# Kernel tuning notes

Hardware: AMD Instinct MI355X
Metric: run time of the kernel (lower is better)

The kernel has to match this reference:

```python
import jax, jax.numpy as jnp
import numpy as np

N_NODES = 50000
N_EDGES = 1_600_000
IN_CH, HID_CH, NUM_CLS = 256, 128, 64
THRESHOLD = 0.5  # default forward arg


def setup_inputs() -> dict:
    key = jax.random.key(0)
    k1, k2, k3, k4 = jax.random.split(key, 4)
    x = jax.random.normal(k1, (N_NODES, IN_CH), dtype=jnp.float32)
    edge_index = jax.random.randint(k2, (2, N_EDGES), 0, N_NODES, dtype=jnp.int32)
    W1 = jax.random.normal(k3, (IN_CH, HID_CH), dtype=jnp.float32) * (1.0 / np.sqrt(IN_CH))
    b1 = jnp.zeros((HID_CH,), dtype=jnp.float32)
    W2 = jax.random.normal(k4, (HID_CH, NUM_CLS), dtype=jnp.float32) * (1.0 / np.sqrt(HID_CH))
    b2 = jnp.zeros((NUM_CLS,), dtype=jnp.float32)
    return {"x": x, "edge_index": edge_index, "W1": W1, "b1": b1, "W2": W2, "b2": b2}


def gcn_conv(x, edge_index, W, b):
    """PyG GCNConv: add self-loops, symmetric D^-1/2 (A+I) D^-1/2 normalization,
    linear transform then gather -> weight -> segment-sum scatter, bias after agg."""
    n = x.shape[0]
    loop = jnp.arange(n, dtype=edge_index.dtype)
    src = jnp.concatenate([edge_index[0], loop])  # message source j
    dst = jnp.concatenate([edge_index[1], loop])  # aggregation target i
    deg = jax.ops.segment_sum(jnp.ones_like(src, dtype=x.dtype), dst, num_segments=n)
    dinv = jnp.where(deg > 0, jax.lax.rsqrt(deg), 0.0)
    norm = dinv[src] * dinv[dst]                  # [E+N]
    h = x @ W                                     # [N, out]
    msg = h[src] * norm[:, None]                  # [E+N, out] gather + scale
    agg = jax.ops.segment_sum(msg, dst, num_segments=n)  # scatter-add
    return agg + b


def reference(x, edge_index, W1, b1, W2, b2):
    h = jax.nn.relu(gcn_conv(x, edge_index, W1, b1))
    logits = gcn_conv(h, edge_index, W2, b2)
    probabilities = jax.nn.sigmoid(logits)
    predictions = (probabilities > THRESHOLD).astype(probabilities.dtype)
    return predictions, probabilities
```

## Files before the change

kernel.cpp:

```cpp
#include <hip/hip_runtime.h>
#include <math.h>

#define EPT 16
#define CHUNK (256 * EPT)
#define CAP 12288


__global__ void bucket_scatter_k(const int* __restrict__ src, const int* __restrict__ dst,
                                 int* __restrict__ bfill, unsigned int* __restrict__ bpk,
                                 int E) {
    __shared__ int hist[256], gofs[256], lfill[256];
    int t = threadIdx.x;
    int base = blockIdx.x * CHUNK;
    hist[t] = 0;
    lfill[t] = 0;
    __syncthreads();
    int ds[EPT], ss[EPT];
#pragma unroll
    for (int i = 0; i < EPT; ++i) {
        int e = base + i * 256 + t;
        if (e < E) {
            ds[i] = dst[e];
            ss[i] = src[e];
            atomicAdd(&hist[ds[i] >> 8], 1);
        } else {
            ds[i] = -1;
        }
    }
    __syncthreads();
    if (hist[t]) gofs[t] = atomicAdd(&bfill[t], hist[t]);
    __syncthreads();
#pragma unroll
    for (int i = 0; i < EPT; ++i) {
        if (ds[i] >= 0) {
            int b = ds[i] >> 8;
            int p = atomicAdd(&lfill[b], 1);
            int idx = gofs[b] + p;
            if (idx < CAP)
                bpk[b * CAP + idx] = ((unsigned)(ds[i] & 255) << 16) | (unsigned)ss[i];
        }
    }
}

__global__ void bucket_build_k(const unsigned int* __restrict__ bpk,
                               const int* __restrict__ bfill,
                               unsigned short* __restrict__ csr,
                               int* __restrict__ rbeg, int* __restrict__ rend,
                               float* __restrict__ dinv, int n) {
    __shared__ int hist[256], loff[256], lfill[256], tmp[256];
    __shared__ unsigned short scsr[CAP];
    int b = blockIdx.x, t = threadIdx.x;
    int base = b * CAP;
    int bsize = min(bfill[b], CAP);
    hist[t] = 0;
    lfill[t] = 0;
    __syncthreads();
    for (int idx = t; idx < bsize; idx += 256)
        atomicAdd(&hist[bpk[base + idx] >> 16], 1);
    __syncthreads();
    int deg = hist[t];
    tmp[t] = deg;
    __syncthreads();
    for (int off = 1; off < 256; off <<= 1) {
        int a = (t >= off) ? tmp[t - off] : 0;
        __syncthreads();
        tmp[t] += a;
        __syncthreads();
    }
    loff[t] = tmp[t] - deg;
    int node = (b << 8) + t;
    if (node < n) {
        rbeg[node] = base + loff[t];
        rend[node] = base + loff[t] + deg;
        dinv[node] = rsqrtf((float)(deg + 1));
    }
    __syncthreads();
    for (int idx = t; idx < bsize; idx += 256) {
        unsigned u = bpk[base + idx];
        int ln = (int)(u >> 16);
        int sp = atomicAdd(&lfill[ln], 1);
        scsr[loff[ln] + sp] = (unsigned short)(u & 0xFFFFu);
    }
    __syncthreads();
    for (int idx = t; idx < bsize; idx += 256)
        csr[base + idx] = scsr[idx];
}


__global__ __launch_bounds__(256) void gemm1_k(const float* __restrict__ x,
                                               const float* __restrict__ W,
                                               const float* __restrict__ dinv,
                                               float* __restrict__ hs, int n) {
    __shared__ float xs[32][32];
    __shared__ float ws[32][128];
    int tid = threadIdx.x;
    int cg = tid & 31;
    int rg = tid >> 5;
    int r0 = blockIdx.x * 32;
    float acc[4][4];
#pragma unroll
    for (int r = 0; r < 4; ++r)
#pragma unroll
        for (int c = 0; c < 4; ++c) acc[r][c] = 0.0f;

    for (int kc = 0; kc < 8; ++kc) {
        __syncthreads();
        {
            int v = tid;
            int r = v >> 3, k4 = v & 7;
            int row = r0 + r;
            float4 val = make_float4(0.f, 0.f, 0.f, 0.f);
            if (row < n) val = *(const float4*)(x + (long long)row * 256 + kc * 32 + k4 * 4);
            *(float4*)&xs[r][k4 * 4] = val;
        }
        {
            const float4* wg = (const float4*)(W + (long long)(kc * 32) * 128);
            float4* wsv = (float4*)&ws[0][0];
#pragma unroll
            for (int v = tid; v < 1024; v += 256) wsv[v] = wg[v];
        }
        __syncthreads();
#pragma unroll
        for (int k4 = 0; k4 < 8; ++k4) {
            float4 w0 = *(const float4*)&ws[k4 * 4 + 0][cg * 4];
            float4 w1 = *(const float4*)&ws[k4 * 4 + 1][cg * 4];
            float4 w2 = *(const float4*)&ws[k4 * 4 + 2][cg * 4];
            float4 w3 = *(const float4*)&ws[k4 * 4 + 3][cg * 4];
#pragma unroll
            for (int r = 0; r < 4; ++r) {
                float4 xv = *(const float4*)&xs[rg * 4 + r][k4 * 4];
                acc[r][0] += xv.x * w0.x + xv.y * w1.x + xv.z * w2.x + xv.w * w3.x;
                acc[r][1] += xv.x * w0.y + xv.y * w1.y + xv.z * w2.y + xv.w * w3.y;
                acc[r][2] += xv.x * w0.z + xv.y * w1.z + xv.z * w2.z + xv.w * w3.z;
                acc[r][3] += xv.x * w0.w + xv.y * w1.w + xv.z * w2.w + xv.w * w3.w;
            }
        }
    }
#pragma unroll
    for (int r = 0; r < 4; ++r) {
        int row = r0 + rg * 4 + r;
        if (row < n) {
            float di = dinv[row];
            float4 o = make_float4(acc[r][0] * di, acc[r][1] * di,
                                   acc[r][2] * di, acc[r][3] * di);
            *(float4*)(hs + (long long)row * 128 + cg * 4) = o;
        }
    }
}


__global__ __launch_bounds__(128) void gemm2_k(const float* __restrict__ h1,
                                               const float* __restrict__ W,
                                               const float* __restrict__ dinv,
                                               float* __restrict__ hs2, int n) {
    __shared__ float xs[32][64];
    int tid = threadIdx.x;
    int cg = tid & 15;
    int rg = tid >> 4;
    int r0 = blockIdx.x * 32;
    float acc[4][4];
#pragma unroll
    for (int r = 0; r < 4; ++r)
#pragma unroll
        for (int c = 0; c < 4; ++c) acc[r][c] = 0.0f;

    for (int kc = 0; kc < 2; ++kc) {
        __syncthreads();
        for (int v = tid; v < 32 * 16; v += 128) {
            int r = v >> 4;
            int k4 = v & 15;
            float4 val = make_float4(0.f, 0.f, 0.f, 0.f);
            int row = r0 + r;
            if (row < n) val = *(const float4*)(h1 + (long long)row * 128 + kc * 64 + k4 * 4);
            *(float4*)&xs[r][k4 * 4] = val;
        }
        __syncthreads();
        const float* Wp = W + (long long)(kc * 64) * 64 + cg * 4;
#pragma unroll 4
        for (int k4 = 0; k4 < 16; ++k4) {
            float4 w0 = *(const float4*)(Wp + (k4 * 4 + 0) * 64);
            float4 w1 = *(const float4*)(Wp + (k4 * 4 + 1) * 64);
            float4 w2 = *(const float4*)(Wp + (k4 * 4 + 2) * 64);
            float4 w3 = *(const float4*)(Wp + (k4 * 4 + 3) * 64);
#pragma unroll
            for (int r = 0; r < 4; ++r) {
                float4 xv = *(const float4*)&xs[rg * 4 + r][k4 * 4];
                acc[r][0] += xv.x * w0.x + xv.y * w1.x + xv.z * w2.x + xv.w * w3.x;
                acc[r][1] += xv.x * w0.y + xv.y * w1.y + xv.z * w2.y + xv.w * w3.y;
                acc[r][2] += xv.x * w0.z + xv.y * w1.z + xv.z * w2.z + xv.w * w3.z;
                acc[r][3] += xv.x * w0.w + xv.y * w1.w + xv.z * w2.w + xv.w * w3.w;
            }
        }
    }
#pragma unroll
    for (int r = 0; r < 4; ++r) {
        int row = r0 + rg * 4 + r;
        if (row < n) {
            float di = dinv[row];
            float4 o = make_float4(acc[r][0] * di, acc[r][1] * di,
                                   acc[r][2] * di, acc[r][3] * di);
            *(float4*)(hs2 + (long long)row * 64 + cg * 4) = o;
        }
    }
}


__global__ void gather1p_k(const float* __restrict__ hs, const int* __restrict__ rbeg,
                           const int* __restrict__ rend, const unsigned short* __restrict__ csr,
                           const float* __restrict__ dinv, const float* __restrict__ b1,
                           float* __restrict__ h1, int n, int gblk) {
    int pass = blockIdx.x / gblk;
    int blk = blockIdx.x - pass * gblk;
    int c0 = pass * 32;
    int g = threadIdx.x >> 3;
    int lane = threadIdx.x & 7;
    int i = blk * 32 + g;
    if (i >= n) return;
    const float* hsc = hs + c0;
    float4 acc = ((const float4*)(hsc + (long long)i * 128))[lane];
    int beg = rbeg[i], end = rend[i];
    int j = beg;
    for (; j + 8 <= end; j += 8) {
        int s0 = csr[j], s1 = csr[j + 1], s2 = csr[j + 2], s3 = csr[j + 3];
        int s4 = csr[j + 4], s5 = csr[j + 5], s6 = csr[j + 6], s7 = csr[j + 7];
        float4 v0 = ((const float4*)(hsc + (long long)s0 * 128))[lane];
        float4 v1 = ((const float4*)(hsc + (long long)s1 * 128))[lane];
        float4 v2 = ((const float4*)(hsc + (long long)s2 * 128))[lane];
        float4 v3 = ((const float4*)(hsc + (long long)s3 * 128))[lane];
        float4 v4 = ((const float4*)(hsc + (long long)s4 * 128))[lane];
        float4 v5 = ((const float4*)(hsc + (long long)s5 * 128))[lane];
        float4 v6 = ((const float4*)(hsc + (long long)s6 * 128))[lane];
        float4 v7 = ((const float4*)(hsc + (long long)s7 * 128))[lane];
        acc.x += (v0.x + v1.x + v2.x + v3.x) + (v4.x + v5.x + v6.x + v7.x);
        acc.y += (v0.y + v1.y + v2.y + v3.y) + (v4.y + v5.y + v6.y + v7.y);
        acc.z += (v0.z + v1.z + v2.z + v3.z) + (v4.z + v5.z + v6.z + v7.z);
        acc.w += (v0.w + v1.w + v2.w + v3.w) + (v4.w + v5.w + v6.w + v7.w);
    }
    for (; j < end; ++j) {
        int s0 = csr[j];
        float4 v0 = ((const float4*)(hsc + (long long)s0 * 128))[lane];
        acc.x += v0.x; acc.y += v0.y; acc.z += v0.z; acc.w += v0.w;
    }
    float di = dinv[i];
    float4 bb = ((const float4*)(b1 + c0))[lane];
    float4 o;
    o.x = fmaxf(di * acc.x + bb.x, 0.0f);
    o.y = fmaxf(di * acc.y + bb.y, 0.0f);
    o.z = fmaxf(di * acc.z + bb.z, 0.0f);
    o.w = fmaxf(di * acc.w + bb.w, 0.0f);
    ((float4*)(h1 + (long long)i * 128 + c0))[lane] = o;
}

__global__ void gather2p_k(const float* __restrict__ hs2, const int* __restrict__ rbeg,
                           const int* __restrict__ rend, const unsigned short* __restrict__ csr,
                           const float* __restrict__ dinv, const float* __restrict__ b2,
                           float* __restrict__ out, int n, int gblk) {
    int pass = blockIdx.x / gblk;
    int blk = blockIdx.x - pass * gblk;
    int c0 = pass * 32;
    int g = threadIdx.x >> 3;
    int lane = threadIdx.x & 7;
    int i = blk * 32 + g;
    if (i >= n) return;
    const float* hc = hs2 + c0;
    float4 acc = ((const float4*)(hc + (long long)i * 64))[lane];
    int beg = rbeg[i], end = rend[i];
    int j = beg;
    for (; j + 8 <= end; j += 8) {
        int s0 = csr[j], s1 = csr[j + 1], s2 = csr[j + 2], s3 = csr[j + 3];
        int s4 = csr[j + 4], s5 = csr[j + 5], s6 = csr[j + 6], s7 = csr[j + 7];
        float4 v0 = ((const float4*)(hc + (long long)s0 * 64))[lane];
        float4 v1 = ((const float4*)(hc + (long long)s1 * 64))[lane];
        float4 v2 = ((const float4*)(hc + (long long)s2 * 64))[lane];
        float4 v3 = ((const float4*)(hc + (long long)s3 * 64))[lane];
        float4 v4 = ((const float4*)(hc + (long long)s4 * 64))[lane];
        float4 v5 = ((const float4*)(hc + (long long)s5 * 64))[lane];
        float4 v6 = ((const float4*)(hc + (long long)s6 * 64))[lane];
        float4 v7 = ((const float4*)(hc + (long long)s7 * 64))[lane];
        acc.x += (v0.x + v1.x + v2.x + v3.x) + (v4.x + v5.x + v6.x + v7.x);
        acc.y += (v0.y + v1.y + v2.y + v3.y) + (v4.y + v5.y + v6.y + v7.y);
        acc.z += (v0.z + v1.z + v2.z + v3.z) + (v4.z + v5.z + v6.z + v7.z);
        acc.w += (v0.w + v1.w + v2.w + v3.w) + (v4.w + v5.w + v6.w + v7.w);
    }
    for (; j < end; ++j) {
        int s0 = csr[j];
        float4 v0 = ((const float4*)(hc + (long long)s0 * 64))[lane];
        acc.x += v0.x; acc.y += v0.y; acc.z += v0.z; acc.w += v0.w;
    }
    float di = dinv[i];
    float4 bb = ((const float4*)(b2 + c0))[lane];
    float lx = di * acc.x + bb.x;
    float ly = di * acc.y + bb.y;
    float lz = di * acc.z + bb.z;
    float lw = di * acc.w + bb.w;
    float4 p;
    p.x = 1.0f / (1.0f + expf(-lx));
    p.y = 1.0f / (1.0f + expf(-ly));
    p.z = 1.0f / (1.0f + expf(-lz));
    p.w = 1.0f / (1.0f + expf(-lw));
    long long total = (long long)n * 64;
    long long o0 = (long long)i * 64 + c0 + lane * 4;
    float4 pr;
    pr.x = (p.x > 0.5f) ? 1.0f : 0.0f;
    pr.y = (p.y > 0.5f) ? 1.0f : 0.0f;
    pr.z = (p.z > 0.5f) ? 1.0f : 0.0f;
    pr.w = (p.w > 0.5f) ? 1.0f : 0.0f;
    *(float4*)(out + o0) = pr;
    *(float4*)(out + total + o0) = p;
}


extern "C" void kernel_launch(void* const* d_in, const int* in_sizes, int n_in,
                              void* d_out, int out_size, void* d_ws, size_t ws_size,
                              hipStream_t stream) {
    const float* x  = (const float*)d_in[0];
    const int*   ei = (const int*)d_in[1];
    const float* W1 = (const float*)d_in[2];
    const float* b1 = (const float*)d_in[3];
    const float* W2 = (const float*)d_in[4];
    const float* b2 = (const float*)d_in[5];
    float* out = (float*)d_out;

    const int n = in_sizes[0] / 256;
    const int E = in_sizes[1] / 2;
    const int* src = ei;
    const int* dst = ei + E;
    const int nb = (n + 255) / 256;

    char* base = (char*)d_ws;
    size_t off = 0;
    auto carve = [&](size_t bytes) -> void* {
        void* p = base + off;
        off = (off + bytes + 255) & ~(size_t)255;
        return p;
    };
    int*   bfill = (int*)  carve(256 * sizeof(int));
    unsigned short* csr = (unsigned short*)carve((size_t)nb * CAP * sizeof(unsigned short));
    int*   rbeg  = (int*)  carve((size_t)n * sizeof(int));
    int*   rend  = (int*)  carve((size_t)n * sizeof(int));
    float* dinv  = (float*)carve((size_t)n * sizeof(float));
    float* hs0   = (float*)carve((size_t)n * 128 * sizeof(float));
    float* h1    = (float*)carve((size_t)n * 128 * sizeof(float));
    float* hs2   = (float*)carve((size_t)n * 64 * sizeof(float));
    unsigned int* bpk = (unsigned int*)hs0;

    hipMemsetAsync(bfill, 0, 256 * sizeof(int), stream);
    bucket_scatter_k<<<(E + CHUNK - 1) / CHUNK, 256, 0, stream>>>(src, dst, bfill, bpk, E);
    bucket_build_k<<<nb, 256, 0, stream>>>(bpk, bfill, csr, rbeg, rend, dinv, n);

    gemm1_k<<<(n + 31) / 32, 256, 0, stream>>>(x, W1, dinv, hs0, n);

    const int gblk = (n + 31) / 32;
    gather1p_k<<<4 * gblk, 256, 0, stream>>>(hs0, rbeg, rend, csr, dinv, b1, h1, n, gblk);

    gemm2_k<<<(n + 31) / 32, 128, 0, stream>>>(h1, W2, dinv, hs2, n);

    gather2p_k<<<2 * gblk, 256, 0, stream>>>(hs2, rbeg, rend, csr, dinv, b2, out, n, gblk);
}
```

Before: 261.0 us.

## Move first GEMM to bf16x3 MFMA with pre-packed split W1

Replaces the FP32 FMA tile loop in the first linear layer with MFMA 16x16x32 bf16 instructions. A new kernel splits W1 into high and low bf16 halves and packs them into the MFMA operand layout. Each x tile is likewise split in shared memory, and three MFMAs (hi*hi, hi*lo, lo*hi) approximate FP32 accuracy. The aim is to cut the ALU cost of the 50k×256×128 GEMM, at the price of an extra small pack launch, a bit of accuracy loss, and scalar (non-vector) output stores.

```diff
diff --git a/kernel.cpp b/kernel.cpp
--- a/kernel.cpp
+++ b/kernel.cpp
@@ -4,6 +4,19 @@
 #define EPT 16
 #define CHUNK (256 * EPT)
 #define CAP 12288
+
+typedef __attribute__((ext_vector_type(8))) short s16x8;
+typedef __attribute__((ext_vector_type(4))) float f32x4;
+
+__device__ inline unsigned short f2bf(float f) {
+    unsigned u = __builtin_bit_cast(unsigned, f);
+    u += 0x7fffu + ((u >> 16) & 1u);
+    return (unsigned short)(u >> 16);
+}
+__device__ inline float bf2f(unsigned short h) {
+    unsigned u = ((unsigned)h) << 16;
+    return __builtin_bit_cast(float, u);
+}
 
 
 __global__ void bucket_scatter_k(const int* __restrict__ src, const int* __restrict__ dst,
@@ -87,63 +100,96 @@
 }
 
 
+__global__ void w1pack_k(const float* __restrict__ W, unsigned short* __restrict__ wh,
+                         unsigned short* __restrict__ wl) {
+    int e = blockIdx.x * 256 + threadIdx.x;
+    int k = e >> 7, col = e & 127;
+    float w = W[e];
+    unsigned short h = f2bf(w);
+    unsigned short l = f2bf(w - bf2f(h));
+    int ct = col >> 4, ks = k >> 5;
+    int lane = (col & 15) + (((k >> 3) & 3) << 4);
+    int i = k & 7;
+    size_t idx = ((((size_t)ct * 8 + ks) * 64 + lane) << 3) + i;
+    wh[idx] = h;
+    wl[idx] = l;
+}
+
+
 __global__ __launch_bounds__(256) void gemm1_k(const float* __restrict__ x,
-                                               const float* __restrict__ W,
+                                               const unsigned short* __restrict__ wh,
+                                               const unsigned short* __restrict__ wl,
                                                const float* __restrict__ dinv,
                                                float* __restrict__ hs, int n) {
-    __shared__ float xs[32][32];
-    __shared__ float ws[32][128];
+    __shared__ __align__(16) unsigned short ah[2 * 8 * 64 * 8];
+    __shared__ __align__(16) unsigned short al[2 * 8 * 64 * 8];
+    __shared__ __align__(16) unsigned short bh[8 * 64 * 8];
+    __shared__ __align__(16) unsigned short bl[8 * 64 * 8];
     int tid = threadIdx.x;
-    int cg = tid & 31;
-    int rg = tid >> 5;
+    int wave = tid >> 6, lane = tid & 63;
+    int band = wave & 1, cq = wave >> 1;
     int r0 = blockIdx.x * 32;
-    float acc[4][4];
-#pragma unroll
-    for (int r = 0; r < 4; ++r)
-#pragma unroll
-        for (int c = 0; c < 4; ++c) acc[r][c] = 0.0f;
-
-    for (int kc = 0; kc < 8; ++kc) {
-        __syncthreads();
-        {
-            int v = tid;
-            int r = v >> 3, k4 = v & 7;
-            int row = r0 + r;
-            float4 val = make_float4(0.f, 0.f, 0.f, 0.f);
-            if (row < n) val = *(const float4*)(x + (long long)row * 256 + kc * 32 + k4 * 4);
-            *(float4*)&xs[r][k4 * 4] = val;
-        }
-        {
-            const float4* wg = (const float4*)(W + (long long)(kc * 32) * 128);
-            float4* wsv = (float4*)&ws[0][0];
-#pragma unroll
-            for (int v = tid; v < 1024; v += 256) wsv[v] = wg[v];
-        }
-        __syncthreads();
-#pragma unroll
-        for (int k4 = 0; k4 < 8; ++k4) {
-            float4 w0 = *(const float4*)&ws[k4 * 4 + 0][cg * 4];
-            float4 w1 = *(const float4*)&ws[k4 * 4 + 1][cg * 4];
-            float4 w2 = *(const float4*)&ws[k4 * 4 + 2][cg * 4];
-            float4 w3 = *(const float4*)&ws[k4 * 4 + 3][cg * 4];
-#pragma unroll
-            for (int r = 0; r < 4; ++r) {
-                float4 xv = *(const float4*)&xs[rg * 4 + r][k4 * 4];
-                acc[r][0] += xv.x * w0.x + xv.y * w1.x + xv.z * w2.x + xv.w * w3.x;
-                acc[r][1] += xv.x * w0.y + xv.y * w1.y + xv.z * w2.y + xv.w * w3.y;
-                acc[r][2] += xv.x * w0.z + xv.y * w1.z + xv.z * w2.z + xv.w * w3.z;
-                acc[r][3] += xv.x * w0.w + xv.y * w1.w + xv.z * w2.w + xv.w * w3.w;
-            }
-        }
-    }
-#pragma unroll
-    for (int r = 0; r < 4; ++r) {
-        int row = r0 + rg * 4 + r;
+
+    for (int v = tid; v < 2048; v += 256) {
+        int r = v >> 6;
+        int k = (v & 63) << 2;
+        int row = r0 + r;
+        if (row >= n) row = n - 1;
+        float4 xv = *(const float4*)(x + (long long)row * 256 + k);
+        int bd = r >> 4, ks = k >> 5;
+        int la = (r & 15) + (((k >> 3) & 3) << 4);
+        int i0 = k & 7;
+        size_t idx = ((((size_t)bd * 8 + ks) * 64 + la) << 3) + i0;
+        ushort4 hh, ll;
+        hh.x = f2bf(xv.x); ll.x = f2bf(xv.x - bf2f(hh.x));
+        hh.y = f2bf(xv.y); ll.y = f2bf(xv.y - bf2f(hh.y));
+        hh.z = f2bf(xv.z); ll.z = f2bf(xv.z - bf2f(hh.z));
+        hh.w = f2bf(xv.w); ll.w = f2bf(xv.w - bf2f(hh.w));
+        *(ushort4*)&ah[idx] = hh;
+        *(ushort4*)&al[idx] = ll;
+    }
+
+    f32x4 acc[4];
+#pragma unroll
+    for (int c = 0; c < 4; ++c) acc[c] = (f32x4){0.f, 0.f, 0.f, 0.f};
+
+    const float4* gh = (const float4*)wh;
+    const float4* gl = (const float4*)wl;
+    for (int ks = 0; ks < 8; ++ks) {
+        __syncthreads();
+#pragma unroll
+        for (int it = 0; it < 2; ++it) {
+            int s = it * 256 + tid;
+            size_t gi = ((size_t)(s >> 6) * 8 + ks) * 64 + (s & 63);
+            ((float4*)bh)[s] = gh[gi];
+            ((float4*)bl)[s] = gl[gi];
+        }
+        __syncthreads();
+        size_t aidx = (((size_t)band * 8 + ks) * 64 + lane) << 3;
+        s16x8 Ah = *(const s16x8*)&ah[aidx];
+        s16x8 Al = *(const s16x8*)&al[aidx];
+#pragma unroll
+        for (int c = 0; c < 4; ++c) {
+            int ct = cq * 4 + c;
+            size_t bidx = (((size_t)ct) * 64 + lane) << 3;
+            s16x8 Bh = *(const s16x8*)&bh[bidx];
+            s16x8 Bl = *(const s16x8*)&bl[bidx];
+            acc[c] = __builtin_amdgcn_mfma_f32_16x16x32_bf16(Ah, Bh, acc[c], 0, 0, 0);
+            acc[c] = __builtin_amdgcn_mfma_f32_16x16x32_bf16(Ah, Bl, acc[c], 0, 0, 0);
+            acc[c] = __builtin_amdgcn_mfma_f32_16x16x32_bf16(Al, Bh, acc[c], 0, 0, 0);
+        }
+    }
+
+    int colb = cq * 64 + (lane & 15);
+    int rbase = r0 + band * 16 + ((lane >> 4) << 2);
+#pragma unroll
+    for (int reg = 0; reg < 4; ++reg) {
+        int row = rbase + reg;
         if (row < n) {
             float di = dinv[row];
-            float4 o = make_float4(acc[r][0] * di, acc[r][1] * di,
-                                   acc[r][2] * di, acc[r][3] * di);
-            *(float4*)(hs + (long long)row * 128 + cg * 4) = o;
+#pragma unroll
+            for (int c = 0; c < 4; ++c)
+                hs[(long long)row * 128 + colb + c * 16] = acc[c][reg] * di;
         }
     }
 }
@@ -339,16 +385,19 @@
     int*   rbeg  = (int*)  carve((size_t)n * sizeof(int));
     int*   rend  = (int*)  carve((size_t)n * sizeof(int));
     float* dinv  = (float*)carve((size_t)n * sizeof(float));
+    unsigned short* w1h = (unsigned short*)carve(32768 * sizeof(unsigned short));
+    unsigned short* w1l = (unsigned short*)carve(32768 * sizeof(unsigned short));
     float* hs0   = (float*)carve((size_t)n * 128 * sizeof(float));
     float* h1    = (float*)carve((size_t)n * 128 * sizeof(float));
     float* hs2   = (float*)carve((size_t)n * 64 * sizeof(float));
     unsigned int* bpk = (unsigned int*)hs0;
 
+    w1pack_k<<<128, 256, 0, stream>>>(W1, w1h, w1l);
     hipMemsetAsync(bfill, 0, 256 * sizeof(int), stream);
     bucket_scatter_k<<<(E + CHUNK - 1) / CHUNK, 256, 0, stream>>>(src, dst, bfill, bpk, E);
     bucket_build_k<<<nb, 256, 0, stream>>>(bpk, bfill, csr, rbeg, rend, dinv, n);
 
-    gemm1_k<<<(n + 31) / 32, 256, 0, stream>>>(x, W1, dinv, hs0, n);
+    gemm1_k<<<(n + 31) / 32, 256, 0, stream>>>(x, w1h, w1l, dinv, hs0, n);
 
     const int gblk = (n + 31) / 32;
     gather1p_k<<<4 * gblk, 256, 0, stream>>>(hs0, rbeg, rend, csr, dinv, b1, h1, n, gblk);
```

Measured after the change: 230.4 us. 11.7% less time.
